# Kernel optimization log

Hardware: AMD Instinct MI355X
Metric: run time of the kernel (lower is better)

The kernel has to match this reference:

```python
import jax, jax.numpy as jnp
import numpy as np
from jax import lax

SPATIAL_K = 30
FEATURE_K = 6
EPS = 1e-12  # F.normalize eps


def setup_inputs() -> dict:
    key = jax.random.key(0)
    k1, k2 = jax.random.split(key)
    N, D = 10000, 256
    ema_feat = jax.random.normal(k1, (N, D), dtype=jnp.float32)
    pos = jax.random.randint(k2, (N, 2), 0, 512, dtype=jnp.int64)
    return {"ema_feat": ema_feat, "pos": pos}


def _spatial_candidates(pos, k_spatial):
    # Brute-force k-NN on 2D integer positions (replaces sklearn KD-tree).
    posf = pos.astype(jnp.float32)  # [N, 2]
    sq = jnp.sum(posf * posf, axis=-1)  # [N]
    d2 = sq[:, None] + sq[None, :] - 2.0 * (posf @ posf.T)  # [N, N]
    N = pos.shape[0]
    # exclude self (sklearn returns self first, code drops column 0)
    d2 = d2 + jnp.where(jnp.eye(N, dtype=bool), jnp.inf, 0.0).astype(d2.dtype)
    _, idx = lax.top_k(-d2, k_spatial)  # nearest = largest negative distance
    return idx  # [N, k_spatial]


def reference(ema_feat, pos):
    N = ema_feat.shape[0]
    k_spatial = min(SPATIAL_K, N - 1)
    k_feat = min(FEATURE_K, k_spatial)

    spatial_candidates = _spatial_candidates(pos, k_spatial)  # [N, Ks]

    # F.normalize(ema_feat, dim=-1): x / max(||x||, eps)
    norm = jnp.linalg.norm(ema_feat, axis=-1, keepdims=True)
    feat_norm = ema_feat / jnp.maximum(norm, EPS)  # [N, D]

    cand_feat = feat_norm[spatial_candidates]  # [N, Ks, D]
    sim = jnp.einsum("nd,nkd->nk", feat_norm, cand_feat)  # cosine sim [N, Ks]

    topk_sim, topk_local_idx = lax.top_k(sim, k_feat)  # [N, Kf]
    topk_indices = jnp.take_along_axis(spatial_candidates, topk_local_idx, axis=1)
    topk_weights = jax.nn.softmax(topk_sim, axis=-1)
    return topk_indices, topk_weights
```

## Files before the change

kernel.cpp:

```cpp
#include <hip/hip_runtime.h>
#include <cstdint>
#include <cstddef>

#define FD    256
#define KS    30
#define KF    6
#define CSH   4
#define GW    32
#define NCELLS (GW*GW)
#define BCAP  40
#define OVCAP 128
#define KREG  8
#define SCAPW 96
#define MAXC  100
#define PIPE  5

#define WFENCE() __threadfence_block()

__global__ __launch_bounds__(1024) void zero_kernel(int* __restrict__ cellCnt,
                                                    int* __restrict__ ovfCnt) {
  cellCnt[threadIdx.x] = 0;
  if (threadIdx.x == 0) *ovfCnt = 0;
}

__global__ __launch_bounds__(256) void prep_bin_kernel(const float* __restrict__ x,
                                                       float* __restrict__ y,
                                                       const int2* __restrict__ pos,
                                                       int* __restrict__ cellCnt,
                                                       int2* __restrict__ bucket,
                                                       int* __restrict__ ovfCnt,
                                                       int2* __restrict__ ovf, int N) {
  const int j = blockIdx.x * 256 + threadIdx.x;
  if (j < N) {
    int2 p = pos[j];
    const int cell = (p.y >> CSH) * GW + (p.x >> CSH);
    const int s = atomicAdd(&cellCnt[cell], 1);
    const int2 e = make_int2(p.x | (p.y << 16), j);
    if (s < BCAP) bucket[cell * BCAP + s] = e;
    else { int o = atomicAdd(ovfCnt, 1); if (o < OVCAP) ovf[o] = e; }
  }
  const int row = blockIdx.x * 4 + (threadIdx.x >> 6);
  if (row >= N) return;
  const int lane = threadIdx.x & 63;
  float4 v = ((const float4*)(x + (size_t)row * FD))[lane];
  float ss = v.x * v.x + v.y * v.y + v.z * v.z + v.w * v.w;
#pragma unroll
  for (int o = 32; o; o >>= 1) ss += __shfl_down(ss, o);
  ss = __shfl(ss, 0);
  const float d = fmaxf(sqrtf(ss), 1e-12f);
  float4 o4;
  o4.x = v.x / d; o4.y = v.y / d; o4.z = v.z / d; o4.w = v.w / d;
  ((float4*)(y + (size_t)row * FD))[lane] = o4;
}

__global__ __launch_bounds__(256, 6) void graph_kernel(const int2* __restrict__ pos,
                                                       const int* __restrict__ cellCnt,
                                                       const int2* __restrict__ bucket,
                                                       const int* __restrict__ ovfCnt,
                                                       const int2* __restrict__ ovf,
                                                       const float* __restrict__ fn,
                                                       float* __restrict__ outI,
                                                       float* __restrict__ outW, int N) {
  __shared__ unsigned long long surv[4][SCAPW];
  __shared__ int pfx[4][MAXC + 1];
  __shared__ int cbase[4][MAXC];
  __shared__ int hist[4][64];
  __shared__ float sims[4][KS];
  __shared__ int selj[4][KS];
  __shared__ int wsel[4][KF];
  __shared__ int kd2[4];

  const int w = threadIdx.x >> 6, lane = threadIdx.x & 63;
  const int qi = blockIdx.x * 4 + w;
  if (qi >= N) return;
  const int ovfN = min(*ovfCnt, OVCAP);

  int i;
  {
    const int4* cc4 = (const int4*)cellCnt;
    int cnts[4][4], lexcl[4], cbases[4];
    int runbase = 0;
#pragma unroll
    for (int c = 0; c < 4; ++c) {
      int4 v = cc4[c * 64 + lane];
      cnts[c][0] = min(v.x, BCAP); cnts[c][1] = min(v.y, BCAP);
      cnts[c][2] = min(v.z, BCAP); cnts[c][3] = min(v.w, BCAP);
      int s = cnts[c][0] + cnts[c][1] + cnts[c][2] + cnts[c][3];
      int incl = s;
#pragma unroll
      for (int o = 1; o < 64; o <<= 1) { int u = __shfl_up(incl, o); if (lane >= o) incl += u; }
      lexcl[c] = incl - s;
      cbases[c] = runbase;
      runbase += __shfl(incl, 63);
    }
    const int total = runbase;
    if (qi < total) {
      int fcell = -1, fslot = 0;
#pragma unroll
      for (int c = 0; c < 4; ++c) {
        int p = cbases[c] + lexcl[c];
#pragma unroll
        for (int k = 0; k < 4; ++k) {
          int cn = cnts[c][k];
          if (qi >= p && qi < p + cn) { fcell = (c * 64 + lane) * 4 + k; fslot = qi - p; }
          p += cn;
        }
      }
      const unsigned long long m = __ballot(fcell >= 0);
      const int src = __ffsll((unsigned long long)m) - 1;
      fcell = __shfl(fcell, src);
      fslot = __shfl(fslot, src);
      i = bucket[fcell * BCAP + fslot].y;
    } else {
      i = ovf[qi - total].y;
    }
  }

  unsigned long long* survw = surv[w];
  int* pfxw = pfx[w];
  int* basew = cbase[w];
  int* histw = hist[w];
  float* simsw = sims[w];
  int* seljw = selj[w];
  int* wselw = wsel[w];

  const int2 q = pos[i];
  const int qx = q.x, qy = q.y;
  const int cx = qx >> CSH, cy = qy >> CSH;

  const float4 q4v = ((const float4*)(fn + (size_t)i * FD))[lane];

  int R = 2;
  int sn = 0;
  for (;;) {
    const int W = 2 * R + 1;
    const int ns = min(W * W, MAXC);
    int run = 0;
    for (int cb = 0; cb < ns; cb += 64) {
      const int s = cb + lane;
      int cnt = 0, base = 0;
      if (s < ns) {
        int dy = s / W - R, dx = s % W - R;
        int yy = cy + dy, xx = cx + dx;
        if (yy >= 0 && yy < GW && xx >= 0 && xx < GW) {
          int cid = yy * GW + xx;
          cnt = min(cellCnt[cid], BCAP);
          base = cid * BCAP;
        }
      }
      int incl = cnt;
#pragma unroll
      for (int o = 1; o < 64; o <<= 1) { int u = __shfl_up(incl, o); if (lane >= o) incl += u; }
      if (s < ns) { pfxw[s] = run + incl - cnt; basew[s] = base; }
      run += __shfl(incl, 63);
    }
    if (lane == 0) pfxw[ns] = run;
    WFENCE();
    const int M = run;
    const int MM = min(M + ovfN, 64 * KREG);

    unsigned long long kreg[KREG];
#pragma unroll
    for (int s8 = 0; s8 < KREG; ++s8) {
      kreg[s8] = ~0ull;
      const int m = lane + 64 * s8;
      if (m < MM) {
        int2 e;
        if (m < M) {
          int c = 0;
#pragma unroll
          for (int st = 64; st; st >>= 1) { int nc = c + st; if (nc < ns && pfxw[nc] <= m) c = nc; }
          e = bucket[basew[c] + (m - pfxw[c])];
        } else {
          e = ovf[m - M];
        }
        const int j = e.y;
        if (j != i) {
          int x = e.x & 0xffff, y = e.x >> 16;
          int dx = qx - x, dy = qy - y;
          unsigned d2 = (unsigned)(dx * dx + dy * dy);
          kreg[s8] = (((unsigned long long)d2) << 16) | (unsigned)j;
        }
      }
    }

    histw[lane] = 0;
    WFENCE();
#pragma unroll
    for (int s8 = 0; s8 < KREG; ++s8)
      if (kreg[s8] != ~0ull)
        atomicAdd(&histw[min((int)(kreg[s8] >> 22), 63)], 1);
    WFENCE();
    int cum = histw[lane];
#pragma unroll
    for (int o = 1; o < 64; o <<= 1) { int u = __shfl_up(cum, o); if (lane >= o) cum += u; }
    const unsigned long long bal = __ballot(cum >= KS);
    unsigned long long Tk;
    if (bal == 0) Tk = 0x7fffffffull << 16;
    else {
      int bb = __ffsll((unsigned long long)bal) - 1;
      Tk = (bb == 63) ? (0x7fffffffull << 16) : (((unsigned long long)(bb + 1) << 6) << 16);
    }

    int sbase = 0;
#pragma unroll
    for (int s8 = 0; s8 < KREG; ++s8) {
      const bool p = kreg[s8] < Tk;
      const unsigned long long mask = __ballot(p);
      if (p) {
        int idx = sbase + __popcll(mask & ((1ull << lane) - 1));
        if (idx < SCAPW) survw[idx] = kreg[s8];
      }
      sbase += __popcll(mask);
    }
    sn = min(sbase, SCAPW);
    WFENCE();

    for (int p = lane; p < sn; p += 64) {
      const unsigned long long kp = survw[p];
      int r = 0;
      for (int s = 0; s < sn; ++s) r += (survw[s] < kp) ? 1 : 0;
      if (r < KS) seljw[r] = (int)(kp & 0xffffu);
      if (r == KS - 1) kd2[w] = (int)(kp >> 16);
    }
    WFENCE();

    bool done = false;
    if (sn >= KS) {
      const int kthd2 = kd2[w];
      int sg = 1 << 15;
      if (cx - R > 0)      sg = min(sg, qx - ((cx - R) << CSH));
      if (cx + R < GW - 1) sg = min(sg, (((cx + R) << CSH) + 15) - qx);
      if (cy - R > 0)      sg = min(sg, qy - ((cy - R) << CSH));
      if (cy + R < GW - 1) sg = min(sg, (((cy + R) << CSH) + 15) - qy);
      done = kthd2 < (sg + 1) * (sg + 1);
    }
    if (done) break;
    ++R;
  }

  float4 fbuf[PIPE];
#pragma unroll
  for (int c = 0; c < PIPE; ++c)
    fbuf[c] = ((const float4*)(fn + (size_t)seljw[c] * FD))[lane];
#pragma unroll
  for (int c = 0; c < KS; ++c) {
    const float4 f = fbuf[c % PIPE];
    if (c + PIPE < KS)
      fbuf[c % PIPE] = ((const float4*)(fn + (size_t)seljw[c + PIPE] * FD))[lane];
    float d = f.x * q4v.x + f.y * q4v.y + f.z * q4v.z + f.w * q4v.w;
#pragma unroll
    for (int o = 32; o; o >>= 1) d += __shfl_down(d, o);
    if (lane == 0) simsw[c] = d;
  }
  WFENCE();

  if (lane < KS) {
    const float simv = simsw[lane];
    int r = 0;
    for (int s = 0; s < KS; ++s) {
      const float so = simsw[s];
      if (so > simv || (so == simv && s < lane)) ++r;
    }
    if (r < KF) wselw[r] = lane;
  }
  WFENCE();

  if (lane < KF) {
    const float m = simsw[wselw[0]];
    float sum = 0.f, my = 0.f;
#pragma unroll
    for (int r = 0; r < KF; ++r) {
      float e = expf(simsw[wselw[r]] - m);
      sum += e;
      if (r == lane) my = e;
    }
    outI[(size_t)i * KF + lane] = (float)seljw[wselw[lane]];
    outW[(size_t)i * KF + lane] = my / sum;
  }
}

extern "C" void kernel_launch(void* const* d_in, const int* in_sizes, int n_in,
                              void* d_out, int out_size, void* d_ws, size_t ws_size,
                              hipStream_t stream) {
  const float* feat = (const float*)d_in[0];
  const int2* pos = (const int2*)d_in[1];
  const int N = in_sizes[1] / 2;

  char* ws = (char*)d_ws;
  float* fn = (float*)ws;
  size_t off = (size_t)N * FD * sizeof(float);
  int* cellCnt = (int*)(ws + off);  off += NCELLS * sizeof(int);
  int* ovfCnt  = (int*)(ws + off);  off += 2 * sizeof(int);
  int2* bucket = (int2*)(ws + off); off += (size_t)NCELLS * BCAP * sizeof(int2);
  int2* ovf    = (int2*)(ws + off); off += OVCAP * sizeof(int2);

  float* out = (float*)d_out;

  zero_kernel<<<1, 1024, 0, stream>>>(cellCnt, ovfCnt);
  prep_bin_kernel<<<(N + 3) / 4, 256, 0, stream>>>(feat, fn, pos, cellCnt, bucket,
                                                   ovfCnt, ovf, N);
  graph_kernel<<<(N + 3) / 4, 256, 0, stream>>>(pos, cellCnt, bucket, ovfCnt, ovf, fn,
                                                out, out + (size_t)N * KF, N);
}
```

Measured before the change: 109.0 us.

## Use DPP wave scans/reductions and XCD-aware block remapping

Replaces shuffle-based 64-lane prefix scans and reductions with DPP row_shr/row_bcast sequences and readlane/readfirstlane broadcasts, avoiding ds_bpermute LDS traffic in the hot loops of the graph kernel and normalization. Also remaps block IDs so consecutive query groups land on the same XCD, aiming to improve L2 locality of bucket and feature reads. Relies on DPP semantics for correctness; remap only changes scheduling.

```diff
diff --git a/kernel.cpp b/kernel.cpp
--- a/kernel.cpp
+++ b/kernel.cpp
@@ -16,6 +16,28 @@
 #define PIPE  5
 
 #define WFENCE() __threadfence_block()
+
+template <int CTRL, int RM, int BM>
+__device__ __forceinline__ int dpp_add_i(int x) {
+  return x + __builtin_amdgcn_update_dpp(0, x, CTRL, RM, BM, false);
+}
+__device__ __forceinline__ int iscan64(int x) {
+  x = dpp_add_i<0x111, 0xF, 0xF>(x);
+  x = dpp_add_i<0x112, 0xF, 0xF>(x);
+  x = dpp_add_i<0x114, 0xF, 0xF>(x);
+  x = dpp_add_i<0x118, 0xF, 0xF>(x);
+  x = dpp_add_i<0x142, 0xA, 0xF>(x);
+  x = dpp_add_i<0x143, 0xC, 0xF>(x);
+  return x;
+}
+template <int CTRL>
+__device__ __forceinline__ float dpp_addf(float x) {
+  int t = __builtin_amdgcn_update_dpp(0, __float_as_int(x), CTRL, 0xF, 0xF, false);
+  return x + __int_as_float(t);
+}
+__device__ __forceinline__ float bcast0_f(float x) {
+  return __int_as_float(__builtin_amdgcn_readfirstlane(__float_as_int(x)));
+}
 
 __global__ __launch_bounds__(1024) void zero_kernel(int* __restrict__ cellCnt,
                                                     int* __restrict__ ovfCnt) {
@@ -44,9 +66,13 @@
   const int lane = threadIdx.x & 63;
   float4 v = ((const float4*)(x + (size_t)row * FD))[lane];
   float ss = v.x * v.x + v.y * v.y + v.z * v.z + v.w * v.w;
-#pragma unroll
-  for (int o = 32; o; o >>= 1) ss += __shfl_down(ss, o);
-  ss = __shfl(ss, 0);
+  ss += __shfl_down(ss, 32);
+  ss += __shfl_down(ss, 16);
+  ss = dpp_addf<0x108>(ss);
+  ss = dpp_addf<0x104>(ss);
+  ss = dpp_addf<0x102>(ss);
+  ss = dpp_addf<0x101>(ss);
+  ss = bcast0_f(ss);
   const float d = fmaxf(sqrtf(ss), 1e-12f);
   float4 o4;
   o4.x = v.x / d; o4.y = v.y / d; o4.z = v.z / d; o4.w = v.w / d;
@@ -71,7 +97,13 @@
   __shared__ int kd2[4];
 
   const int w = threadIdx.x >> 6, lane = threadIdx.x & 63;
-  const int qi = blockIdx.x * 4 + w;
+
+  const int nwg = gridDim.x, orig = blockIdx.x;
+  const int qq = nwg >> 3, rr = nwg & 7;
+  const int xcd = orig & 7, idx = orig >> 3;
+  const int bid = (xcd < rr ? xcd * (qq + 1) : rr * (qq + 1) + (xcd - rr) * qq) + idx;
+
+  const int qi = bid * 4 + w;
   if (qi >= N) return;
   const int ovfN = min(*ovfCnt, OVCAP);
 
@@ -86,12 +118,10 @@
       cnts[c][0] = min(v.x, BCAP); cnts[c][1] = min(v.y, BCAP);
       cnts[c][2] = min(v.z, BCAP); cnts[c][3] = min(v.w, BCAP);
       int s = cnts[c][0] + cnts[c][1] + cnts[c][2] + cnts[c][3];
-      int incl = s;
-#pragma unroll
-      for (int o = 1; o < 64; o <<= 1) { int u = __shfl_up(incl, o); if (lane >= o) incl += u; }
+      int incl = iscan64(s);
       lexcl[c] = incl - s;
       cbases[c] = runbase;
-      runbase += __shfl(incl, 63);
+      runbase += __builtin_amdgcn_readlane(incl, 63);
     }
     const int total = runbase;
     if (qi < total) {
@@ -108,8 +138,8 @@
       }
       const unsigned long long m = __ballot(fcell >= 0);
       const int src = __ffsll((unsigned long long)m) - 1;
-      fcell = __shfl(fcell, src);
-      fslot = __shfl(fslot, src);
+      fcell = __builtin_amdgcn_readlane(fcell, src);
+      fslot = __builtin_amdgcn_readlane(fslot, src);
       i = bucket[fcell * BCAP + fslot].y;
     } else {
       i = ovf[qi - total].y;
@@ -148,11 +178,9 @@
           base = cid * BCAP;
         }
       }
-      int incl = cnt;
-#pragma unroll
-      for (int o = 1; o < 64; o <<= 1) { int u = __shfl_up(incl, o); if (lane >= o) incl += u; }
+      int incl = iscan64(cnt);
       if (s < ns) { pfxw[s] = run + incl - cnt; basew[s] = base; }
-      run += __shfl(incl, 63);
+      run += __builtin_amdgcn_readlane(incl, 63);
     }
     if (lane == 0) pfxw[ns] = run;
     WFENCE();
@@ -191,9 +219,7 @@
       if (kreg[s8] != ~0ull)
         atomicAdd(&histw[min((int)(kreg[s8] >> 22), 63)], 1);
     WFENCE();
-    int cum = histw[lane];
-#pragma unroll
-    for (int o = 1; o < 64; o <<= 1) { int u = __shfl_up(cum, o); if (lane >= o) cum += u; }
+    int cum = iscan64(histw[lane]);
     const unsigned long long bal = __ballot(cum >= KS);
     unsigned long long Tk;
     if (bal == 0) Tk = 0x7fffffffull << 16;
@@ -208,8 +234,8 @@
       const bool p = kreg[s8] < Tk;
       const unsigned long long mask = __ballot(p);
       if (p) {
-        int idx = sbase + __popcll(mask & ((1ull << lane) - 1));
-        if (idx < SCAPW) survw[idx] = kreg[s8];
+        int idx2 = sbase + __popcll(mask & ((1ull << lane) - 1));
+        if (idx2 < SCAPW) survw[idx2] = kreg[s8];
       }
       sbase += __popcll(mask);
     }
@@ -249,8 +275,12 @@
     if (c + PIPE < KS)
       fbuf[c % PIPE] = ((const float4*)(fn + (size_t)seljw[c + PIPE] * FD))[lane];
     float d = f.x * q4v.x + f.y * q4v.y + f.z * q4v.z + f.w * q4v.w;
-#pragma unroll
-    for (int o = 32; o; o >>= 1) d += __shfl_down(d, o);
+    d += __shfl_down(d, 32);
+    d += __shfl_down(d, 16);
+    d = dpp_addf<0x108>(d);
+    d = dpp_addf<0x104>(d);
+    d = dpp_addf<0x102>(d);
+    d = dpp_addf<0x101>(d);
     if (lane == 0) simsw[c] = d;
   }
   WFENCE();
```

Measured after the change: 98.07 us. 10.0% less time.
